# Optimization experiments

Measured on AMD Instinct MI355X. Metric: run time of the kernel, lower is better.

## Reference

```python
import jax, jax.numpy as jnp
import numpy as np

B, S, NL, VMAX = 16, 256, 66, 8
CORE_IDX = jnp.array([1, 2, 3, 4, 5, 6])  # indices of B-A0..B-A5 core role labels
EYE_BIG = 1e4   # matches torch.eye(orig_l) * 10000 self-exclusion mask
PAD_BIG = 1e9   # excludes tokens beyond orig_l from the min (orig code slices them off)
CLAMP_MIN = 1e-6


def setup_inputs() -> dict:
    key = jax.random.key(0)
    k1, k2, k3, k4 = jax.random.split(key, 4)
    logits = jax.random.normal(k1, (B, S, S, NL), dtype=jnp.float32)
    # log_pa are per-token label log-probabilities (output of log_softmax upstream)
    log_pa = jax.nn.log_softmax(logits, axis=-1)
    v_label = jax.random.randint(k2, (B, VMAX), 0, S)          # predicate positions
    v_l = jax.random.randint(k3, (B,), 1, VMAX + 1)            # num predicates per ex
    orig_l = jax.random.randint(k4, (B,), S // 2, S + 1)       # true sequence lengths
    return {"log_pa": log_pa, "v_label": v_label, "v_l": v_l, "orig_l": orig_l}


def reference(log_pa, v_label, v_l, orig_l):
    dt = log_pa.dtype
    # gather predicate rows: [B, Vmax, S, NL] -> core labels only: [B, Vmax, S, C]
    log_core = jnp.take_along_axis(log_pa, v_label[:, :, None, None], axis=1)
    log_core = log_core[..., CORE_IDX]
    # log(1 - p) with clamp, per (predicate, token, core-label)
    log_neg = jnp.log(jnp.clip(1.0 - jnp.exp(log_core), CLAMP_MIN))  # [B, V, S, C]

    tok = jnp.arange(S)
    tok_invalid = tok[None, :] >= orig_l[:, None]                    # [B, S] pads
    eye_mask = jnp.eye(S, dtype=dt) * EYE_BIG                        # [Sj, St]
    pad_mask = tok_invalid.astype(dt) * PAD_BIG                      # [B, St]

    # expanded [B, V, Sj, St, C]: min over other tokens t for each position j
    neg_ext = (log_neg[:, :, None, :, :]
               + eye_mask[None, None, :, :, None]
               + pad_mask[:, None, None, :, None])
    min_neg = jnp.min(neg_ext, axis=3)                               # [B, V, Sj, C]

    term = jax.nn.relu(log_core - min_neg)                           # [B, V, Sj, C]
    # validity: real predicates (v < v_l) and real tokens (j < orig_l)
    v_valid = (jnp.arange(VMAX)[None, :] < v_l[:, None]).astype(dt)  # [B, V]
    j_valid = (~tok_invalid).astype(dt)                              # [B, Sj]
    w = v_valid[:, :, None, None] * j_valid[:, None, :, None]

    loss = jnp.sum(term * w)
    normalizer = jnp.sum(v_l).astype(dt)  # use_gold_predicate == 1 branch
    return loss / normalizer
```

## Files before the change

kernel.cpp:

```cpp
#include <hip/hip_runtime.h>

#define BB 16
#define SS 256
#define NLL 66
#define VMAXX 8
#define CC 6
#define CLAMP_MIN 1e-6f
#define NB2 32
#define WPB 4

__global__ __launch_bounds__(256)
void urloss_one(const float* __restrict__ log_pa,
                const int* __restrict__ v_label,
                const int* __restrict__ v_l,
                const int* __restrict__ orig_l,
                double* __restrict__ slot,
                unsigned long long* __restrict__ counter,
                float* __restrict__ out) {
    const int tid  = threadIdx.x;
    const int lane = tid & 63;
    const int wid  = tid >> 6;
    const int blk  = blockIdx.x;
    const int pair = blk * WPB + wid;
    const int b = pair >> 3;
    const int v = pair & 7;

    __shared__ float wsum[WPB][CC];

    float sc[CC];
#pragma unroll
    for (int c = 0; c < CC; ++c) sc[c] = 0.0f;

    if (v < v_l[b]) {
        const int p    = v_label[b * VMAXX + v];
        const int orig = orig_l[b];
        const size_t rowbase = (size_t)(b * SS + p) * SS;

        float vals[4][CC];
        float m1[CC], m2[CC];
        int   ix[CC];
#pragma unroll
        for (int c = 0; c < CC; ++c) { m1[c] = 1e30f; m2[c] = 1e30f; ix[c] = -1; }

#pragma unroll
        for (int k = 0; k < 4; ++k) {
            const int t = lane + 64 * k;
            const float2* r2 = (const float2*)log_pa + (rowbase + t) * (NLL / 2);
            const float2 a0 = r2[0], a1 = r2[1], a2 = r2[2], a3 = r2[3];
            vals[k][0] = a0.y;  vals[k][1] = a1.x;  vals[k][2] = a1.y;
            vals[k][3] = a2.x;  vals[k][4] = a2.y;  vals[k][5] = a3.x;
            if (t < orig) {
#pragma unroll
                for (int c = 0; c < CC; ++c) {
                    const float ln = logf(fmaxf(1.0f - expf(vals[k][c]), CLAMP_MIN));
                    if (ln < m1[c]) { m2[c] = m1[c]; m1[c] = ln; ix[c] = t; }
                    else if (ln < m2[c]) { m2[c] = ln; }
                }
            }
        }

#pragma unroll
        for (int off = 32; off >= 1; off >>= 1) {
#pragma unroll
            for (int c = 0; c < CC; ++c) {
                const float o1 = __shfl_down(m1[c], off);
                const float o2 = __shfl_down(m2[c], off);
                const int   oi = __shfl_down(ix[c], off);
                if (o1 < m1[c]) { m2[c] = fminf(m1[c], o2); m1[c] = o1; ix[c] = oi; }
                else            { m2[c] = fminf(m2[c], o1); }
            }
        }
#pragma unroll
        for (int c = 0; c < CC; ++c) {
            m1[c] = __shfl(m1[c], 0);
            m2[c] = __shfl(m2[c], 0);
            ix[c] = __shfl(ix[c], 0);
        }

#pragma unroll
        for (int k = 0; k < 4; ++k) {
            const int t = lane + 64 * k;
            if (t < orig) {
#pragma unroll
                for (int c = 0; c < CC; ++c) {
                    const float sel = (t == ix[c]) ? m2[c] : m1[c];
                    sc[c] += fmaxf(vals[k][c] - sel, 0.0f);
                }
            }
        }
#pragma unroll
        for (int off = 32; off >= 1; off >>= 1)
#pragma unroll
            for (int c = 0; c < CC; ++c)
                sc[c] += __shfl_down(sc[c], off);
    }

    if (lane == 0)
#pragma unroll
        for (int c = 0; c < CC; ++c) wsum[wid][c] = sc[c];
    __syncthreads();
    if (wid != 0) return;

    unsigned long long old = 0;
    if (lane == 0) {
        double bsum = 0.0;
        for (int w = 0; w < WPB; ++w)
            for (int c = 0; c < CC; ++c)
                bsum += (double)wsum[w][c];
        __hip_atomic_store(&slot[blk], bsum,
                           __ATOMIC_RELEASE, __HIP_MEMORY_SCOPE_AGENT);
        old = __hip_atomic_fetch_add(counter, 1ull,
                                     __ATOMIC_ACQ_REL, __HIP_MEMORY_SCOPE_AGENT);
    }
    old = __shfl(old, 0);
    if (old % (unsigned long long)NB2 != (unsigned long long)(NB2 - 1)) return;

    double d = (lane < NB2)
        ? __hip_atomic_load(&slot[lane], __ATOMIC_RELAXED, __HIP_MEMORY_SCOPE_AGENT)
        : 0.0;
#pragma unroll
    for (int off = 32; off >= 1; off >>= 1)
        d += __shfl_down(d, off);

    if (lane == 0) {
        int norm = 0;
        for (int bb = 0; bb < BB; ++bb) norm += v_l[bb];
        out[0] = (float)(d / (double)norm);
    }
}

extern "C" void kernel_launch(void* const* d_in, const int* in_sizes, int n_in,
                              void* d_out, int out_size, void* d_ws, size_t ws_size,
                              hipStream_t stream) {
    const float* log_pa  = (const float*)d_in[0];
    const int*   v_label = (const int*)d_in[1];
    const int*   v_l     = (const int*)d_in[2];
    const int*   orig_l  = (const int*)d_in[3];
    double* slot = (double*)d_ws;
    unsigned long long* counter = (unsigned long long*)((char*)d_ws + NB2 * sizeof(double));

    urloss_one<<<NB2, 256, 0, stream>>>(log_pa, v_label, v_l, orig_l,
                                        slot, counter, (float*)d_out);
}
```

Measured before the change: 14.34 us.

## Track max log-prob before transform; split into per-pair blocks plus reduce kernel

Because log(1-exp(x)) is monotonically decreasing, the kernel now tracks the top-two raw log-probabilities per core label and applies the log/exp transform only to those two values, instead of to every token. It also replaces the 32-block, 4-wave kernel with one 64-thread block per (batch, predicate) pair that writes a partial sum to a slot. A second single-block kernel then reduces the slots, replacing the atomic counter and last-block finalization. The extra launch adds launch overhead, which may outweigh the saved transcendental math and atomics for such a small kernel.

```diff
diff --git a/kernel.cpp b/kernel.cpp
--- a/kernel.cpp
+++ b/kernel.cpp
@@ -6,127 +6,117 @@
 #define VMAXX 8
 #define CC 6
 #define CLAMP_MIN 1e-6f
-#define NB2 32
-#define WPB 4
+#define NPAIR (BB * VMAXX)
 
-__global__ __launch_bounds__(256)
-void urloss_one(const float* __restrict__ log_pa,
-                const int* __restrict__ v_label,
-                const int* __restrict__ v_l,
-                const int* __restrict__ orig_l,
-                double* __restrict__ slot,
-                unsigned long long* __restrict__ counter,
-                float* __restrict__ out) {
-    const int tid  = threadIdx.x;
-    const int lane = tid & 63;
-    const int wid  = tid >> 6;
-    const int blk  = blockIdx.x;
-    const int pair = blk * WPB + wid;
+
+__global__ __launch_bounds__(64)
+void urloss_pairs(const float* __restrict__ log_pa,
+                  const int* __restrict__ v_label,
+                  const int* __restrict__ v_l,
+                  const int* __restrict__ orig_l,
+                  double* __restrict__ slot) {
+    const int pair = blockIdx.x;
     const int b = pair >> 3;
     const int v = pair & 7;
+    const int lane = threadIdx.x;
 
-    __shared__ float wsum[WPB][CC];
+    if (v >= v_l[b]) {
+        if (lane == 0) slot[pair] = 0.0;
+        return;
+    }
+    const int p    = v_label[b * VMAXX + v];
+    const int orig = orig_l[b];
+    const size_t rowbase = (size_t)(b * SS + p) * SS;
+
+    float vals[4][CC];
+    float M1[CC], M2[CC];
+    int   ix[CC];
+#pragma unroll
+    for (int c = 0; c < CC; ++c) { M1[c] = -1e30f; M2[c] = -1e30f; ix[c] = -1; }
+
+#pragma unroll
+    for (int k = 0; k < 4; ++k) {
+        const int t = lane + 64 * k;
+        const float2* r2 = (const float2*)log_pa + (rowbase + t) * (NLL / 2);
+        const float2 a0 = r2[0], a1 = r2[1], a2 = r2[2], a3 = r2[3];
+        vals[k][0] = a0.y;  vals[k][1] = a1.x;  vals[k][2] = a1.y;
+        vals[k][3] = a2.x;  vals[k][4] = a2.y;  vals[k][5] = a3.x;
+        if (t < orig) {
+#pragma unroll
+            for (int c = 0; c < CC; ++c) {
+                const float lc = vals[k][c];
+                if (lc > M1[c]) { M2[c] = M1[c]; M1[c] = lc; ix[c] = t; }
+                else            { M2[c] = fmaxf(M2[c], lc); }
+            }
+        }
+    }
+
+#pragma unroll
+    for (int off = 32; off >= 1; off >>= 1) {
+#pragma unroll
+        for (int c = 0; c < CC; ++c) {
+            const float o1 = __shfl_down(M1[c], off);
+            const float o2 = __shfl_down(M2[c], off);
+            const int   oi = __shfl_down(ix[c], off);
+            if (o1 > M1[c]) { M2[c] = fmaxf(M1[c], o2); M1[c] = o1; ix[c] = oi; }
+            else            { M2[c] = fmaxf(M2[c], o1); }
+        }
+    }
+#pragma unroll
+    for (int c = 0; c < CC; ++c) {
+        M1[c] = __shfl(M1[c], 0);
+        M2[c] = __shfl(M2[c], 0);
+        ix[c] = __shfl(ix[c], 0);
+    }
+
+    float mn1[CC], mn2[CC];
+#pragma unroll
+    for (int c = 0; c < CC; ++c) {
+        mn1[c] = logf(fmaxf(1.0f - expf(M1[c]), CLAMP_MIN));
+        mn2[c] = logf(fmaxf(1.0f - expf(M2[c]), CLAMP_MIN));
+    }
 
     float sc[CC];
 #pragma unroll
     for (int c = 0; c < CC; ++c) sc[c] = 0.0f;
-
-    if (v < v_l[b]) {
-        const int p    = v_label[b * VMAXX + v];
-        const int orig = orig_l[b];
-        const size_t rowbase = (size_t)(b * SS + p) * SS;
-
-        float vals[4][CC];
-        float m1[CC], m2[CC];
-        int   ix[CC];
 #pragma unroll
-        for (int c = 0; c < CC; ++c) { m1[c] = 1e30f; m2[c] = 1e30f; ix[c] = -1; }
-
+    for (int k = 0; k < 4; ++k) {
+        const int t = lane + 64 * k;
+        if (t < orig) {
 #pragma unroll
-        for (int k = 0; k < 4; ++k) {
-            const int t = lane + 64 * k;
-            const float2* r2 = (const float2*)log_pa + (rowbase + t) * (NLL / 2);
-            const float2 a0 = r2[0], a1 = r2[1], a2 = r2[2], a3 = r2[3];
-            vals[k][0] = a0.y;  vals[k][1] = a1.x;  vals[k][2] = a1.y;
-            vals[k][3] = a2.x;  vals[k][4] = a2.y;  vals[k][5] = a3.x;
-            if (t < orig) {
-#pragma unroll
-                for (int c = 0; c < CC; ++c) {
-                    const float ln = logf(fmaxf(1.0f - expf(vals[k][c]), CLAMP_MIN));
-                    if (ln < m1[c]) { m2[c] = m1[c]; m1[c] = ln; ix[c] = t; }
-                    else if (ln < m2[c]) { m2[c] = ln; }
-                }
+            for (int c = 0; c < CC; ++c) {
+                const float sel = (t == ix[c]) ? mn2[c] : mn1[c];
+                sc[c] += fmaxf(vals[k][c] - sel, 0.0f);
             }
         }
-
-#pragma unroll
-        for (int off = 32; off >= 1; off >>= 1) {
-#pragma unroll
-            for (int c = 0; c < CC; ++c) {
-                const float o1 = __shfl_down(m1[c], off);
-                const float o2 = __shfl_down(m2[c], off);
-                const int   oi = __shfl_down(ix[c], off);
-                if (o1 < m1[c]) { m2[c] = fminf(m1[c], o2); m1[c] = o1; ix[c] = oi; }
-                else            { m2[c] = fminf(m2[c], o1); }
-            }
-        }
-#pragma unroll
-        for (int c = 0; c < CC; ++c) {
-            m1[c] = __shfl(m1[c], 0);
-            m2[c] = __shfl(m2[c], 0);
-            ix[c] = __shfl(ix[c], 0);
-        }
-
-#pragma unroll
-        for (int k = 0; k < 4; ++k) {
-            const int t = lane + 64 * k;
-            if (t < orig) {
-#pragma unroll
-                for (int c = 0; c < CC; ++c) {
-                    const float sel = (t == ix[c]) ? m2[c] : m1[c];
-                    sc[c] += fmaxf(vals[k][c] - sel, 0.0f);
-                }
-            }
-        }
-#pragma unroll
-        for (int off = 32; off >= 1; off >>= 1)
-#pragma unroll
-            for (int c = 0; c < CC; ++c)
-                sc[c] += __shfl_down(sc[c], off);
     }
-
-    if (lane == 0)
-#pragma unroll
-        for (int c = 0; c < CC; ++c) wsum[wid][c] = sc[c];
-    __syncthreads();
-    if (wid != 0) return;
-
-    unsigned long long old = 0;
-    if (lane == 0) {
-        double bsum = 0.0;
-        for (int w = 0; w < WPB; ++w)
-            for (int c = 0; c < CC; ++c)
-                bsum += (double)wsum[w][c];
-        __hip_atomic_store(&slot[blk], bsum,
-                           __ATOMIC_RELEASE, __HIP_MEMORY_SCOPE_AGENT);
-        old = __hip_atomic_fetch_add(counter, 1ull,
-                                     __ATOMIC_ACQ_REL, __HIP_MEMORY_SCOPE_AGENT);
-    }
-    old = __shfl(old, 0);
-    if (old % (unsigned long long)NB2 != (unsigned long long)(NB2 - 1)) return;
-
-    double d = (lane < NB2)
-        ? __hip_atomic_load(&slot[lane], __ATOMIC_RELAXED, __HIP_MEMORY_SCOPE_AGENT)
-        : 0.0;
 #pragma unroll
     for (int off = 32; off >= 1; off >>= 1)
-        d += __shfl_down(d, off);
+#pragma unroll
+        for (int c = 0; c < CC; ++c)
+            sc[c] += __shfl_down(sc[c], off);
 
     if (lane == 0) {
-        int norm = 0;
-        for (int bb = 0; bb < BB; ++bb) norm += v_l[bb];
-        out[0] = (float)(d / (double)norm);
+        double d = 0.0;
+#pragma unroll
+        for (int c = 0; c < CC; ++c) d += (double)sc[c];
+        slot[pair] = d;
     }
+}
+
+__global__ __launch_bounds__(64)
+void urloss_reduce(const double* __restrict__ slot,
+                   const int* __restrict__ v_l,
+                   float* __restrict__ out) {
+    const int lane = threadIdx.x;
+    double s = slot[lane] + slot[lane + 64];
+    int nv = (lane < BB) ? v_l[lane] : 0;
+#pragma unroll
+    for (int off = 32; off >= 1; off >>= 1) {
+        s  += __shfl_down(s, off);
+        nv += __shfl_down(nv, off);
+    }
+    if (lane == 0) out[0] = (float)(s / (double)nv);
 }
 
 extern "C" void kernel_launch(void* const* d_in, const int* in_sizes, int n_in,
@@ -137,8 +127,7 @@
     const int*   v_l     = (const int*)d_in[2];
     const int*   orig_l  = (const int*)d_in[3];
     double* slot = (double*)d_ws;
-    unsigned long long* counter = (unsigned long long*)((char*)d_ws + NB2 * sizeof(double));
 
-    urloss_one<<<NB2, 256, 0, stream>>>(log_pa, v_label, v_l, orig_l,
-                                        slot, counter, (float*)d_out);
+    urloss_pairs<<<NPAIR, 64, 0, stream>>>(log_pa, v_label, v_l, orig_l, slot);
+    urloss_reduce<<<1, 64, 0, stream>>>(slot, v_l, (float*)d_out);
 }
```

New measurement: 12.80 us. 10.8% less time.
